# Optimization experiments

Measured on AMD Instinct MI355X. Metric: run time of the kernel, lower is better.

The kernel has to match this reference:

```python
import jax, jax.numpy as jnp
import numpy as np

NUM_CLASSES = 19  # number of distinct labels in targets (fill_max)


def setup_inputs() -> dict:
    key = jax.random.key(0)
    k1, k2 = jax.random.split(key)
    n, d = 262144, 128
    inputs = jax.random.normal(k1, (n, d), dtype=jnp.float32)
    targets = jax.random.randint(k2, (n,), 0, NUM_CLASSES, dtype=jnp.int64)
    return {"inputs": inputs, "targets": targets}


def reference(inputs, targets):
    # Same math as the O(n^2) torch loop: for each sample i, the center is the
    # mean of all samples sharing targets[i]. Computed as one segment-reduction
    # over labels followed by a gather.
    n = inputs.shape[0]
    sums = jax.ops.segment_sum(inputs, targets, num_segments=NUM_CLASSES)          # [C, d]
    counts = jax.ops.segment_sum(jnp.ones((n,), inputs.dtype), targets,
                                 num_segments=NUM_CLASSES)                          # [C]
    class_centers = sums / counts[:, None]                                          # [C, d]
    centers = class_centers[targets]                                                # [n, d]
    dist_pc = jnp.sqrt(jnp.sum((inputs - centers) ** 2, axis=1))                    # [n]
    return jnp.mean(dist_pc)
```

## Files before the change

kernel.cpp:

```cpp
#include <hip/hip_runtime.h>
#include <math.h>

#define NCLS 19
#define DIM  128
#define CD   (NCLS * DIM)
#define WPB  8
#define NBLK 256
#define NTHR 512
#define NWAVES (NBLK * WPB)
#define NRP  32

typedef float f32x4 __attribute__((ext_vector_type(4)));

__device__ __forceinline__ float4 ntload4(const float4* p) {
    f32x4 r = __builtin_nontemporal_load((const f32x4*)p);
    return make_float4(r.x, r.y, r.z, r.w);
}

template <int CTRL, int RMASK>
__device__ __forceinline__ float dpp_add(float x) {
    int t = __builtin_amdgcn_update_dpp(0, __builtin_bit_cast(int, x),
                                        CTRL, RMASK, 0xf, true);
    return x + __builtin_bit_cast(float, t);
}
__device__ __forceinline__ float reduce32_dpp(float x) {
    x = dpp_add<0x111, 0xf>(x);
    x = dpp_add<0x112, 0xf>(x);
    x = dpp_add<0x114, 0xf>(x);
    x = dpp_add<0x118, 0xf>(x);
    x = dpp_add<0x142, 0xa>(x);
    return x;
}

__device__ __forceinline__ void proc_pair(float* __restrict__ tbl,
                                          int* __restrict__ cnt,
                                          float4 v, int ca, int cb,
                                          int lane, int l31) {
    if (ca == cb) {
        v.x += __shfl_xor(v.x, 32, 64);
        v.y += __shfl_xor(v.y, 32, 64);
        v.z += __shfl_xor(v.z, 32, 64);
        v.w += __shfl_xor(v.w, 32, 64);
        float4* q = (float4*)&tbl[ca * DIM + l31 * 4];
        float4 a = *q;
        a.x += v.x; a.y += v.y; a.z += v.z; a.w += v.w;
        *q = a;
        if (lane == 0) cnt[ca] += 2;
    } else {
        int c = (lane >= 32) ? cb : ca;
        float4* q = (float4*)&tbl[c * DIM + l31 * 4];
        float4 a = *q;
        a.x += v.x; a.y += v.y; a.z += v.z; a.w += v.w;
        *q = a;
        if (lane == 0)  cnt[ca]++;
        if (lane == 32) cnt[cb]++;
    }
}

__global__ __launch_bounds__(NTHR, 2)
void k_fused(const float4* __restrict__ in4, const int* __restrict__ tgt,
             float* __restrict__ gsums, int* __restrict__ gcounts,
             int* __restrict__ bar, float* __restrict__ out,
             int npair, float inv_n) {
    __shared__ __align__(16) float ls[WPB * CD];
    __shared__ int   lcnt[WPB * NCLS];
    __shared__ __align__(16) float lcent[CD];
    __shared__ float red[NTHR];

    const int tid  = threadIdx.x;
    const int w    = tid >> 6;
    const int lane = tid & 63;
    const int l31  = lane & 31;
    float* tbl = &ls[w * CD];
    int*   cnt = &lcnt[w * NCLS];
    const int g = blockIdx.x * WPB + w;

    for (int i = tid; i < WPB * CD; i += NTHR) ls[i] = 0.0f;
    for (int i = tid; i < WPB * NCLS; i += NTHR) lcnt[i] = 0;
    __syncthreads();

    const int hstop = (npair >= NRP * NWAVES) ? NRP * NWAVES : 0;
    const bool full = hstop != 0;

    float4 hold[NRP];
    if (full) {
        #pragma unroll
        for (int k = 0; k < NRP; k += 4) {
            const int p0 = (k + 0) * NWAVES + g;
            const int p1 = (k + 1) * NWAVES + g;
            const int p2 = (k + 2) * NWAVES + g;
            const int p3 = (k + 3) * NWAVES + g;
            float4 v0 = ntload4(&in4[(size_t)p0 * 64 + lane]);
            float4 v1 = ntload4(&in4[(size_t)p1 * 64 + lane]);
            float4 v2 = ntload4(&in4[(size_t)p2 * 64 + lane]);
            float4 v3 = ntload4(&in4[(size_t)p3 * 64 + lane]);
            hold[k + 0] = v0; hold[k + 1] = v1;
            hold[k + 2] = v2; hold[k + 3] = v3;
            int a0 = tgt[2 * p0];  int b0 = tgt[2 * p0 + 1];
            int a1 = tgt[2 * p1];  int b1 = tgt[2 * p1 + 1];
            int a2 = tgt[2 * p2];  int b2 = tgt[2 * p2 + 1];
            int a3 = tgt[2 * p3];  int b3 = tgt[2 * p3 + 1];
            proc_pair(tbl, cnt, v0, a0, b0, lane, l31);
            proc_pair(tbl, cnt, v1, a1, b1, lane, l31);
            proc_pair(tbl, cnt, v2, a2, b2, lane, l31);
            proc_pair(tbl, cnt, v3, a3, b3, lane, l31);
        }
        #pragma unroll
        for (int k = 0; k < NRP; k++) {
            asm volatile("" : "+v"(hold[k].x), "+v"(hold[k].y),
                              "+v"(hold[k].z), "+v"(hold[k].w));
        }
    }

    int p = hstop + g;
    for (; p + 3 * NWAVES < npair; p += 4 * NWAVES) {
        float4 v0 = in4[(size_t)(p             ) * 64 + lane];
        float4 v1 = in4[(size_t)(p +     NWAVES) * 64 + lane];
        float4 v2 = in4[(size_t)(p + 2 * NWAVES) * 64 + lane];
        float4 v3 = in4[(size_t)(p + 3 * NWAVES) * 64 + lane];
        int a0 = tgt[2 * p];                  int b0 = tgt[2 * p + 1];
        int a1 = tgt[2 * (p + NWAVES)];       int b1 = tgt[2 * (p + NWAVES) + 1];
        int a2 = tgt[2 * (p + 2 * NWAVES)];   int b2 = tgt[2 * (p + 2 * NWAVES) + 1];
        int a3 = tgt[2 * (p + 3 * NWAVES)];   int b3 = tgt[2 * (p + 3 * NWAVES) + 1];
        proc_pair(tbl, cnt, v0, a0, b0, lane, l31);
        proc_pair(tbl, cnt, v1, a1, b1, lane, l31);
        proc_pair(tbl, cnt, v2, a2, b2, lane, l31);
        proc_pair(tbl, cnt, v3, a3, b3, lane, l31);
    }
    for (; p < npair; p += NWAVES) {
        float4 v = in4[(size_t)p * 64 + lane];
        int ca = tgt[2 * p];
        int cb = tgt[2 * p + 1];
        proc_pair(tbl, cnt, v, ca, cb, lane, l31);
    }
    __syncthreads();

    for (int i = tid; i < CD; i += NTHR) {
        float s = 0.0f;
        #pragma unroll
        for (int ww = 0; ww < WPB; ww++) s += ls[ww * CD + i];
        unsafeAtomicAdd(&gsums[i], s);
    }
    if (tid < NCLS) {
        int s = 0;
        #pragma unroll
        for (int ww = 0; ww < WPB; ww++) s += lcnt[ww * NCLS + tid];
        atomicAdd(&gcounts[tid], s);
    }

    __syncthreads();
    if (tid == 0) {
        __hip_atomic_fetch_add(bar, 1, __ATOMIC_ACQ_REL,
                               __HIP_MEMORY_SCOPE_AGENT);
        while (__hip_atomic_load(bar, __ATOMIC_ACQUIRE,
                                 __HIP_MEMORY_SCOPE_AGENT) < NBLK) {
            __builtin_amdgcn_s_sleep(8);
        }
    }
    __syncthreads();

    for (int i = tid; i < CD; i += NTHR) {
        float s = __hip_atomic_load(&gsums[i], __ATOMIC_RELAXED,
                                    __HIP_MEMORY_SCOPE_AGENT);
        int   c = __hip_atomic_load(&gcounts[i >> 7], __ATOMIC_RELAXED,
                                    __HIP_MEMORY_SCOPE_AGENT);
        lcent[i] = s / (float)c;
    }
    __syncthreads();

    float acc = 0.0f;

    if (full) {
        #pragma unroll
        for (int k = 0; k < NRP; k++) {
            const int pk = k * NWAVES + g;
            const int2 cc = *(const int2*)&tgt[2 * pk];
            const int c = (lane >= 32) ? cc.y : cc.x;
            const float4 e = *(const float4*)&lcent[c * DIM + l31 * 4];
            const float4 v = hold[k];
            float dx = v.x - e.x, dy = v.y - e.y;
            float dz = v.z - e.z, dw = v.w - e.w;
            float d = dx * dx + dy * dy + dz * dz + dw * dw;
            d = reduce32_dpp(d);
            if (l31 == 31) acc += sqrtf(d);
        }
    }

    int q = hstop + g;
    for (; q + NWAVES < npair; q += 2 * NWAVES) {
        float4 va = in4[(size_t)q * 64 + lane];
        float4 vb = in4[(size_t)(q + NWAVES) * 64 + lane];
        int2 c2a = *(const int2*)&tgt[2 * q];
        int2 c2b = *(const int2*)&tgt[2 * (q + NWAVES)];
        int ca = (lane >= 32) ? c2a.y : c2a.x;
        int cb = (lane >= 32) ? c2b.y : c2b.x;
        float4 ea = *(const float4*)&lcent[ca * DIM + l31 * 4];
        float4 eb = *(const float4*)&lcent[cb * DIM + l31 * 4];
        float dx, dy, dz, dw;
        dx = va.x - ea.x; dy = va.y - ea.y; dz = va.z - ea.z; dw = va.w - ea.w;
        float d0 = dx * dx + dy * dy + dz * dz + dw * dw;
        dx = vb.x - eb.x; dy = vb.y - eb.y; dz = vb.z - eb.z; dw = vb.w - eb.w;
        float d1 = dx * dx + dy * dy + dz * dz + dw * dw;
        d0 = reduce32_dpp(d0);
        d1 = reduce32_dpp(d1);
        if (l31 == 31) acc += sqrtf(d0) + sqrtf(d1);
    }
    for (; q < npair; q += NWAVES) {
        float4 v = in4[(size_t)q * 64 + lane];
        int2 c2 = *(const int2*)&tgt[2 * q];
        int c = (lane >= 32) ? c2.y : c2.x;
        float4 e = *(const float4*)&lcent[c * DIM + l31 * 4];
        float dx = v.x - e.x, dy = v.y - e.y, dz = v.z - e.z, dw = v.w - e.w;
        float d = dx * dx + dy * dy + dz * dz + dw * dw;
        d = reduce32_dpp(d);
        if (l31 == 31) acc += sqrtf(d);
    }

    red[tid] = acc;
    __syncthreads();
    for (int s = NTHR / 2; s > 0; s >>= 1) {
        if (tid < s) red[tid] += red[tid + s];
        __syncthreads();
    }
    if (tid == 0) unsafeAtomicAdd(out, red[0] * inv_n);
}

extern "C" void kernel_launch(void* const* d_in, const int* in_sizes, int n_in,
                              void* d_out, int out_size, void* d_ws, size_t ws_size,
                              hipStream_t stream) {
    const float* in  = (const float*)d_in[0];
    const int*   tgt = (const int*)d_in[1];
    const int n = in_sizes[0] / DIM;

    float* gsums   = (float*)d_ws;
    int*   gcounts = (int*)(gsums + CD);
    int*   bar     = gcounts + NCLS;
    float* out     = (float*)d_out;

    (void)hipMemsetAsync(d_ws, 0, (CD + NCLS + 1) * sizeof(float), stream);
    (void)hipMemsetAsync(d_out, 0, sizeof(float), stream);

    const float4* in4 = (const float4*)in;
    k_fused<<<NBLK, NTHR, 0, stream>>>(in4, tgt, gsums, gcounts, bar,
                                       out, n / 2, 1.0f / (float)n);
}
```

Before: 230.1 us.

## Share one LDS atomic table per block and cache extra pairs in LDS

Replaces the eight per-wave shared class-sum tables with one block-wide table updated by LDS float atomics. This removes the cross-wave merge step and frees shared memory. The freed space, plus more, holds 16 extra row-pairs per wave in LDS between the accumulation and distance phases, so the second pass rereads less input from global memory. Lanes now write to the sum table with a strided column layout, and the distance phase reads it back the same way. The costs are atomic contention on the shared table, more LDS instructions per pair, and about 150 KB of shared memory per block, which caps residency at one block per CU.

```diff
diff --git a/kernel.cpp b/kernel.cpp
--- a/kernel.cpp
+++ b/kernel.cpp
@@ -9,6 +9,8 @@
 #define NTHR 512
 #define NWAVES (NBLK * WPB)
 #define NRP  32
+#define NLP  16
+#define PPW  64
 
 typedef float f32x4 __attribute__((ext_vector_type(4)));
 
@@ -32,29 +34,27 @@
     return x;
 }
 
-__device__ __forceinline__ void proc_pair(float* __restrict__ tbl,
-                                          int* __restrict__ cnt,
-                                          float4 v, int ca, int cb,
-                                          int lane, int l31) {
-    if (ca == cb) {
-        v.x += __shfl_xor(v.x, 32, 64);
-        v.y += __shfl_xor(v.y, 32, 64);
-        v.z += __shfl_xor(v.z, 32, 64);
-        v.w += __shfl_xor(v.w, 32, 64);
-        float4* q = (float4*)&tbl[ca * DIM + l31 * 4];
-        float4 a = *q;
-        a.x += v.x; a.y += v.y; a.z += v.z; a.w += v.w;
-        *q = a;
-        if (lane == 0) cnt[ca] += 2;
-    } else {
-        int c = (lane >= 32) ? cb : ca;
-        float4* q = (float4*)&tbl[c * DIM + l31 * 4];
-        float4 a = *q;
-        a.x += v.x; a.y += v.y; a.z += v.z; a.w += v.w;
-        *q = a;
-        if (lane == 0)  cnt[ca]++;
-        if (lane == 32) cnt[cb]++;
-    }
+__device__ __forceinline__ void acc_pair(float* __restrict__ tbl,
+                                         int* __restrict__ cnt,
+                                         float4 v, int ca, int cb,
+                                         int lane, int l31) {
+    const int c = (lane >= 32) ? cb : ca;
+    float* row = &tbl[c * DIM];
+    atomicAdd(&row[l31     ], v.x);
+    atomicAdd(&row[l31 + 32], v.y);
+    atomicAdd(&row[l31 + 64], v.z);
+    atomicAdd(&row[l31 + 96], v.w);
+    if (l31 == 0) atomicAdd(&cnt[c], 1);
+}
+
+__device__ __forceinline__ float pair_dist2(const float* __restrict__ lcent,
+                                            float4 v, int c, int l31) {
+    const float* row = &lcent[c * DIM];
+    float dx = v.x - row[l31     ];
+    float dy = v.y - row[l31 + 32];
+    float dz = v.z - row[l31 + 64];
+    float dw = v.w - row[l31 + 96];
+    return dx * dx + dy * dy + dz * dz + dw * dw;
 }
 
 __global__ __launch_bounds__(NTHR, 2)
@@ -62,28 +62,27 @@
              float* __restrict__ gsums, int* __restrict__ gcounts,
              int* __restrict__ bar, float* __restrict__ out,
              int npair, float inv_n) {
-    __shared__ __align__(16) float ls[WPB * CD];
-    __shared__ int   lcnt[WPB * NCLS];
+    __shared__ __align__(16) float tbl[CD];
     __shared__ __align__(16) float lcent[CD];
+    __shared__ int   cnt[NCLS];
     __shared__ float red[NTHR];
+    __shared__ __align__(16) float4 holdl[WPB * NLP * 64];
 
     const int tid  = threadIdx.x;
     const int w    = tid >> 6;
     const int lane = tid & 63;
     const int l31  = lane & 31;
-    float* tbl = &ls[w * CD];
-    int*   cnt = &lcnt[w * NCLS];
-    const int g = blockIdx.x * WPB + w;
-
-    for (int i = tid; i < WPB * CD; i += NTHR) ls[i] = 0.0f;
-    for (int i = tid; i < WPB * NCLS; i += NTHR) lcnt[i] = 0;
-    __syncthreads();
-
-    const int hstop = (npair >= NRP * NWAVES) ? NRP * NWAVES : 0;
-    const bool full = hstop != 0;
+    const int g    = blockIdx.x * WPB + w;
+
+    for (int i = tid; i < CD; i += NTHR) tbl[i] = 0.0f;
+    if (tid < NCLS) cnt[tid] = 0;
+    __syncthreads();
+
+    const bool exact = (npair == PPW * NWAVES);
+    const int  lstop = exact ? (NRP + NLP) * NWAVES : 0;
 
     float4 hold[NRP];
-    if (full) {
+    if (exact) {
         #pragma unroll
         for (int k = 0; k < NRP; k += 4) {
             const int p0 = (k + 0) * NWAVES + g;
@@ -94,59 +93,75 @@
             float4 v1 = ntload4(&in4[(size_t)p1 * 64 + lane]);
             float4 v2 = ntload4(&in4[(size_t)p2 * 64 + lane]);
             float4 v3 = ntload4(&in4[(size_t)p3 * 64 + lane]);
+            int2 ab0 = *(const int2*)&tgt[2 * p0];
+            int2 ab1 = *(const int2*)&tgt[2 * p1];
+            int2 ab2 = *(const int2*)&tgt[2 * p2];
+            int2 ab3 = *(const int2*)&tgt[2 * p3];
             hold[k + 0] = v0; hold[k + 1] = v1;
             hold[k + 2] = v2; hold[k + 3] = v3;
-            int a0 = tgt[2 * p0];  int b0 = tgt[2 * p0 + 1];
-            int a1 = tgt[2 * p1];  int b1 = tgt[2 * p1 + 1];
-            int a2 = tgt[2 * p2];  int b2 = tgt[2 * p2 + 1];
-            int a3 = tgt[2 * p3];  int b3 = tgt[2 * p3 + 1];
-            proc_pair(tbl, cnt, v0, a0, b0, lane, l31);
-            proc_pair(tbl, cnt, v1, a1, b1, lane, l31);
-            proc_pair(tbl, cnt, v2, a2, b2, lane, l31);
-            proc_pair(tbl, cnt, v3, a3, b3, lane, l31);
+            acc_pair(tbl, cnt, v0, ab0.x, ab0.y, lane, l31);
+            acc_pair(tbl, cnt, v1, ab1.x, ab1.y, lane, l31);
+            acc_pair(tbl, cnt, v2, ab2.x, ab2.y, lane, l31);
+            acc_pair(tbl, cnt, v3, ab3.x, ab3.y, lane, l31);
         }
         #pragma unroll
         for (int k = 0; k < NRP; k++) {
             asm volatile("" : "+v"(hold[k].x), "+v"(hold[k].y),
                               "+v"(hold[k].z), "+v"(hold[k].w));
         }
-    }
-
-    int p = hstop + g;
+
+        float4* hbase = &holdl[(size_t)(w * NLP) * 64 + lane];
+        #pragma unroll
+        for (int k = 0; k < NLP; k += 4) {
+            const int p0 = (NRP + k + 0) * NWAVES + g;
+            const int p1 = (NRP + k + 1) * NWAVES + g;
+            const int p2 = (NRP + k + 2) * NWAVES + g;
+            const int p3 = (NRP + k + 3) * NWAVES + g;
+            float4 v0 = ntload4(&in4[(size_t)p0 * 64 + lane]);
+            float4 v1 = ntload4(&in4[(size_t)p1 * 64 + lane]);
+            float4 v2 = ntload4(&in4[(size_t)p2 * 64 + lane]);
+            float4 v3 = ntload4(&in4[(size_t)p3 * 64 + lane]);
+            int2 ab0 = *(const int2*)&tgt[2 * p0];
+            int2 ab1 = *(const int2*)&tgt[2 * p1];
+            int2 ab2 = *(const int2*)&tgt[2 * p2];
+            int2 ab3 = *(const int2*)&tgt[2 * p3];
+            hbase[(k + 0) * 64] = v0;
+            hbase[(k + 1) * 64] = v1;
+            hbase[(k + 2) * 64] = v2;
+            hbase[(k + 3) * 64] = v3;
+            acc_pair(tbl, cnt, v0, ab0.x, ab0.y, lane, l31);
+            acc_pair(tbl, cnt, v1, ab1.x, ab1.y, lane, l31);
+            acc_pair(tbl, cnt, v2, ab2.x, ab2.y, lane, l31);
+            acc_pair(tbl, cnt, v3, ab3.x, ab3.y, lane, l31);
+        }
+    }
+
+    int p = lstop + g;
     for (; p + 3 * NWAVES < npair; p += 4 * NWAVES) {
         float4 v0 = in4[(size_t)(p             ) * 64 + lane];
         float4 v1 = in4[(size_t)(p +     NWAVES) * 64 + lane];
         float4 v2 = in4[(size_t)(p + 2 * NWAVES) * 64 + lane];
         float4 v3 = in4[(size_t)(p + 3 * NWAVES) * 64 + lane];
-        int a0 = tgt[2 * p];                  int b0 = tgt[2 * p + 1];
-        int a1 = tgt[2 * (p + NWAVES)];       int b1 = tgt[2 * (p + NWAVES) + 1];
-        int a2 = tgt[2 * (p + 2 * NWAVES)];   int b2 = tgt[2 * (p + 2 * NWAVES) + 1];
-        int a3 = tgt[2 * (p + 3 * NWAVES)];   int b3 = tgt[2 * (p + 3 * NWAVES) + 1];
-        proc_pair(tbl, cnt, v0, a0, b0, lane, l31);
-        proc_pair(tbl, cnt, v1, a1, b1, lane, l31);
-        proc_pair(tbl, cnt, v2, a2, b2, lane, l31);
-        proc_pair(tbl, cnt, v3, a3, b3, lane, l31);
+        int2 ab0 = *(const int2*)&tgt[2 * p];
+        int2 ab1 = *(const int2*)&tgt[2 * (p + NWAVES)];
+        int2 ab2 = *(const int2*)&tgt[2 * (p + 2 * NWAVES)];
+        int2 ab3 = *(const int2*)&tgt[2 * (p + 3 * NWAVES)];
+        acc_pair(tbl, cnt, v0, ab0.x, ab0.y, lane, l31);
+        acc_pair(tbl, cnt, v1, ab1.x, ab1.y, lane, l31);
+        acc_pair(tbl, cnt, v2, ab2.x, ab2.y, lane, l31);
+        acc_pair(tbl, cnt, v3, ab3.x, ab3.y, lane, l31);
     }
     for (; p < npair; p += NWAVES) {
         float4 v = in4[(size_t)p * 64 + lane];
-        int ca = tgt[2 * p];
-        int cb = tgt[2 * p + 1];
-        proc_pair(tbl, cnt, v, ca, cb, lane, l31);
-    }
-    __syncthreads();
-
-    for (int i = tid; i < CD; i += NTHR) {
-        float s = 0.0f;
-        #pragma unroll
-        for (int ww = 0; ww < WPB; ww++) s += ls[ww * CD + i];
-        unsafeAtomicAdd(&gsums[i], s);
-    }
-    if (tid < NCLS) {
-        int s = 0;
-        #pragma unroll
-        for (int ww = 0; ww < WPB; ww++) s += lcnt[ww * NCLS + tid];
-        atomicAdd(&gcounts[tid], s);
-    }
+        int2 ab = *(const int2*)&tgt[2 * p];
+        acc_pair(tbl, cnt, v, ab.x, ab.y, lane, l31);
+    }
+    __syncthreads();
+
+    for (int i = tid; i < CD; i += NTHR)
+        unsafeAtomicAdd(&gsums[i], tbl[i]);
+    if (tid < NCLS)
+        atomicAdd(&gcounts[tid], cnt[tid]);
 
     __syncthreads();
     if (tid == 0) {
@@ -170,23 +185,30 @@
 
     float acc = 0.0f;
 
-    if (full) {
+    if (exact) {
         #pragma unroll
         for (int k = 0; k < NRP; k++) {
             const int pk = k * NWAVES + g;
             const int2 cc = *(const int2*)&tgt[2 * pk];
             const int c = (lane >= 32) ? cc.y : cc.x;
-            const float4 e = *(const float4*)&lcent[c * DIM + l31 * 4];
-            const float4 v = hold[k];
-            float dx = v.x - e.x, dy = v.y - e.y;
-            float dz = v.z - e.z, dw = v.w - e.w;
-            float d = dx * dx + dy * dy + dz * dz + dw * dw;
+            float d = pair_dist2(lcent, hold[k], c, l31);
             d = reduce32_dpp(d);
             if (l31 == 31) acc += sqrtf(d);
         }
-    }
-
-    int q = hstop + g;
+        const float4* hbase = &holdl[(size_t)(w * NLP) * 64 + lane];
+        #pragma unroll
+        for (int k = 0; k < NLP; k++) {
+            const int pk = (NRP + k) * NWAVES + g;
+            const int2 cc = *(const int2*)&tgt[2 * pk];
+            const int c = (lane >= 32) ? cc.y : cc.x;
+            float4 v = hbase[k * 64];
+            float d = pair_dist2(lcent, v, c, l31);
+            d = reduce32_dpp(d);
+            if (l31 == 31) acc += sqrtf(d);
+        }
+    }
+
+    int q = lstop + g;
     for (; q + NWAVES < npair; q += 2 * NWAVES) {
         float4 va = in4[(size_t)q * 64 + lane];
         float4 vb = in4[(size_t)(q + NWAVES) * 64 + lane];
@@ -194,13 +216,8 @@
         int2 c2b = *(const int2*)&tgt[2 * (q + NWAVES)];
         int ca = (lane >= 32) ? c2a.y : c2a.x;
         int cb = (lane >= 32) ? c2b.y : c2b.x;
-        float4 ea = *(const float4*)&lcent[ca * DIM + l31 * 4];
-        float4 eb = *(const float4*)&lcent[cb * DIM + l31 * 4];
-        float dx, dy, dz, dw;
-        dx = va.x - ea.x; dy = va.y - ea.y; dz = va.z - ea.z; dw = va.w - ea.w;
-        float d0 = dx * dx + dy * dy + dz * dz + dw * dw;
-        dx = vb.x - eb.x; dy = vb.y - eb.y; dz = vb.z - eb.z; dw = vb.w - eb.w;
-        float d1 = dx * dx + dy * dy + dz * dz + dw * dw;
+        float d0 = pair_dist2(lcent, va, ca, l31);
+        float d1 = pair_dist2(lcent, vb, cb, l31);
         d0 = reduce32_dpp(d0);
         d1 = reduce32_dpp(d1);
         if (l31 == 31) acc += sqrtf(d0) + sqrtf(d1);
@@ -209,9 +226,7 @@
         float4 v = in4[(size_t)q * 64 + lane];
         int2 c2 = *(const int2*)&tgt[2 * q];
         int c = (lane >= 32) ? c2.y : c2.x;
-        float4 e = *(const float4*)&lcent[c * DIM + l31 * 4];
-        float dx = v.x - e.x, dy = v.y - e.y, dz = v.z - e.z, dw = v.w - e.w;
-        float d = dx * dx + dy * dy + dz * dz + dw * dw;
+        float d = pair_dist2(lcent, v, c, l31);
         d = reduce32_dpp(d);
         if (l31 == 31) acc += sqrtf(d);
     }
```

Result: slower. 359.1 us (+56.1%).

## Stage extra input rows in LDS to cut second-pass global rereads

Applied to the files above, without the earlier changes.

Adds an LDS buffer holding 8 more pairs per wave beyond the 32 kept in registers, so 40 of the 64 pairs per wave skip the second global read after the grid barrier. To make room, the class-center table now reuses the per-wave sums LDS region instead of a separate array. Target labels are loaded as int2 pairs. The register/LDS path only runs when npair exactly matches the expected size, and the larger LDS footprint may reduce occupancy below 2 blocks per CU.

```diff
diff --git a/kernel.cpp b/kernel.cpp
--- a/kernel.cpp
+++ b/kernel.cpp
@@ -9,6 +9,8 @@
 #define NTHR 512
 #define NWAVES (NBLK * WPB)
 #define NRP  32
+#define NLP  8
+#define PPW  64
 
 typedef float f32x4 __attribute__((ext_vector_type(4)));
 
@@ -64,8 +66,8 @@
              int npair, float inv_n) {
     __shared__ __align__(16) float ls[WPB * CD];
     __shared__ int   lcnt[WPB * NCLS];
-    __shared__ __align__(16) float lcent[CD];
     __shared__ float red[NTHR];
+    __shared__ __align__(16) float4 holdl[WPB * NLP * 64];
 
     const int tid  = threadIdx.x;
     const int w    = tid >> 6;
@@ -79,11 +81,11 @@
     for (int i = tid; i < WPB * NCLS; i += NTHR) lcnt[i] = 0;
     __syncthreads();
 
-    const int hstop = (npair >= NRP * NWAVES) ? NRP * NWAVES : 0;
-    const bool full = hstop != 0;
+    const bool exact = (npair == PPW * NWAVES);
+    const int  lstop = exact ? (NRP + NLP) * NWAVES : 0;
 
     float4 hold[NRP];
-    if (full) {
+    if (exact) {
         #pragma unroll
         for (int k = 0; k < NRP; k += 4) {
             const int p0 = (k + 0) * NWAVES + g;
@@ -94,44 +96,68 @@
             float4 v1 = ntload4(&in4[(size_t)p1 * 64 + lane]);
             float4 v2 = ntload4(&in4[(size_t)p2 * 64 + lane]);
             float4 v3 = ntload4(&in4[(size_t)p3 * 64 + lane]);
+            int2 ab0 = *(const int2*)&tgt[2 * p0];
+            int2 ab1 = *(const int2*)&tgt[2 * p1];
+            int2 ab2 = *(const int2*)&tgt[2 * p2];
+            int2 ab3 = *(const int2*)&tgt[2 * p3];
             hold[k + 0] = v0; hold[k + 1] = v1;
             hold[k + 2] = v2; hold[k + 3] = v3;
-            int a0 = tgt[2 * p0];  int b0 = tgt[2 * p0 + 1];
-            int a1 = tgt[2 * p1];  int b1 = tgt[2 * p1 + 1];
-            int a2 = tgt[2 * p2];  int b2 = tgt[2 * p2 + 1];
-            int a3 = tgt[2 * p3];  int b3 = tgt[2 * p3 + 1];
-            proc_pair(tbl, cnt, v0, a0, b0, lane, l31);
-            proc_pair(tbl, cnt, v1, a1, b1, lane, l31);
-            proc_pair(tbl, cnt, v2, a2, b2, lane, l31);
-            proc_pair(tbl, cnt, v3, a3, b3, lane, l31);
+            proc_pair(tbl, cnt, v0, ab0.x, ab0.y, lane, l31);
+            proc_pair(tbl, cnt, v1, ab1.x, ab1.y, lane, l31);
+            proc_pair(tbl, cnt, v2, ab2.x, ab2.y, lane, l31);
+            proc_pair(tbl, cnt, v3, ab3.x, ab3.y, lane, l31);
         }
         #pragma unroll
         for (int k = 0; k < NRP; k++) {
             asm volatile("" : "+v"(hold[k].x), "+v"(hold[k].y),
                               "+v"(hold[k].z), "+v"(hold[k].w));
         }
-    }
-
-    int p = hstop + g;
+
+        float4* hbase = &holdl[(size_t)(w * NLP) * 64 + lane];
+        #pragma unroll
+        for (int k = 0; k < NLP; k += 4) {
+            const int p0 = (NRP + k + 0) * NWAVES + g;
+            const int p1 = (NRP + k + 1) * NWAVES + g;
+            const int p2 = (NRP + k + 2) * NWAVES + g;
+            const int p3 = (NRP + k + 3) * NWAVES + g;
+            float4 v0 = ntload4(&in4[(size_t)p0 * 64 + lane]);
+            float4 v1 = ntload4(&in4[(size_t)p1 * 64 + lane]);
+            float4 v2 = ntload4(&in4[(size_t)p2 * 64 + lane]);
+            float4 v3 = ntload4(&in4[(size_t)p3 * 64 + lane]);
+            int2 ab0 = *(const int2*)&tgt[2 * p0];
+            int2 ab1 = *(const int2*)&tgt[2 * p1];
+            int2 ab2 = *(const int2*)&tgt[2 * p2];
+            int2 ab3 = *(const int2*)&tgt[2 * p3];
+            hbase[(k + 0) * 64] = v0;
+            hbase[(k + 1) * 64] = v1;
+            hbase[(k + 2) * 64] = v2;
+            hbase[(k + 3) * 64] = v3;
+            proc_pair(tbl, cnt, v0, ab0.x, ab0.y, lane, l31);
+            proc_pair(tbl, cnt, v1, ab1.x, ab1.y, lane, l31);
+            proc_pair(tbl, cnt, v2, ab2.x, ab2.y, lane, l31);
+            proc_pair(tbl, cnt, v3, ab3.x, ab3.y, lane, l31);
+        }
+    }
+
+    int p = lstop + g;
     for (; p + 3 * NWAVES < npair; p += 4 * NWAVES) {
         float4 v0 = in4[(size_t)(p             ) * 64 + lane];
         float4 v1 = in4[(size_t)(p +     NWAVES) * 64 + lane];
         float4 v2 = in4[(size_t)(p + 2 * NWAVES) * 64 + lane];
         float4 v3 = in4[(size_t)(p + 3 * NWAVES) * 64 + lane];
-        int a0 = tgt[2 * p];                  int b0 = tgt[2 * p + 1];
-        int a1 = tgt[2 * (p + NWAVES)];       int b1 = tgt[2 * (p + NWAVES) + 1];
-        int a2 = tgt[2 * (p + 2 * NWAVES)];   int b2 = tgt[2 * (p + 2 * NWAVES) + 1];
-        int a3 = tgt[2 * (p + 3 * NWAVES)];   int b3 = tgt[2 * (p + 3 * NWAVES) + 1];
-        proc_pair(tbl, cnt, v0, a0, b0, lane, l31);
-        proc_pair(tbl, cnt, v1, a1, b1, lane, l31);
-        proc_pair(tbl, cnt, v2, a2, b2, lane, l31);
-        proc_pair(tbl, cnt, v3, a3, b3, lane, l31);
+        int2 ab0 = *(const int2*)&tgt[2 * p];
+        int2 ab1 = *(const int2*)&tgt[2 * (p + NWAVES)];
+        int2 ab2 = *(const int2*)&tgt[2 * (p + 2 * NWAVES)];
+        int2 ab3 = *(const int2*)&tgt[2 * (p + 3 * NWAVES)];
+        proc_pair(tbl, cnt, v0, ab0.x, ab0.y, lane, l31);
+        proc_pair(tbl, cnt, v1, ab1.x, ab1.y, lane, l31);
+        proc_pair(tbl, cnt, v2, ab2.x, ab2.y, lane, l31);
+        proc_pair(tbl, cnt, v3, ab3.x, ab3.y, lane, l31);
     }
     for (; p < npair; p += NWAVES) {
         float4 v = in4[(size_t)p * 64 + lane];
-        int ca = tgt[2 * p];
-        int cb = tgt[2 * p + 1];
-        proc_pair(tbl, cnt, v, ca, cb, lane, l31);
+        int2 ab = *(const int2*)&tgt[2 * p];
+        proc_pair(tbl, cnt, v, ab.x, ab.y, lane, l31);
     }
     __syncthreads();
 
@@ -159,6 +185,7 @@
     }
     __syncthreads();
 
+    float* lcent = ls;
     for (int i = tid; i < CD; i += NTHR) {
         float s = __hip_atomic_load(&gsums[i], __ATOMIC_RELAXED,
                                     __HIP_MEMORY_SCOPE_AGENT);
@@ -170,7 +197,7 @@
 
     float acc = 0.0f;
 
-    if (full) {
+    if (exact) {
         #pragma unroll
         for (int k = 0; k < NRP; k++) {
             const int pk = k * NWAVES + g;
@@ -184,9 +211,23 @@
             d = reduce32_dpp(d);
             if (l31 == 31) acc += sqrtf(d);
         }
-    }
-
-    int q = hstop + g;
+        const float4* hbase = &holdl[(size_t)(w * NLP) * 64 + lane];
+        #pragma unroll
+        for (int k = 0; k < NLP; k++) {
+            const int pk = (NRP + k) * NWAVES + g;
+            const int2 cc = *(const int2*)&tgt[2 * pk];
+            const int c = (lane >= 32) ? cc.y : cc.x;
+            float4 v = hbase[k * 64];
+            const float4 e = *(const float4*)&lcent[c * DIM + l31 * 4];
+            float dx = v.x - e.x, dy = v.y - e.y;
+            float dz = v.z - e.z, dw = v.w - e.w;
+            float d = dx * dx + dy * dy + dz * dz + dw * dw;
+            d = reduce32_dpp(d);
+            if (l31 == 31) acc += sqrtf(d);
+        }
+    }
+
+    int q = lstop + g;
     for (; q + NWAVES < npair; q += 2 * NWAVES) {
         float4 va = in4[(size_t)q * 64 + lane];
         float4 vb = in4[(size_t)(q + NWAVES) * 64 + lane];
@@ -194,8 +235,8 @@
         int2 c2b = *(const int2*)&tgt[2 * (q + NWAVES)];
         int ca = (lane >= 32) ? c2a.y : c2a.x;
         int cb = (lane >= 32) ? c2b.y : c2b.x;
-        float4 ea = *(const float4*)&lcent[ca * DIM + l31 * 4];
-        float4 eb = *(const float4*)&lcent[cb * DIM + l31 * 4];
+        const float4 ea = *(const float4*)&lcent[ca * DIM + l31 * 4];
+        const float4 eb = *(const float4*)&lcent[cb * DIM + l31 * 4];
         float dx, dy, dz, dw;
         dx = va.x - ea.x; dy = va.y - ea.y; dz = va.z - ea.z; dw = va.w - ea.w;
         float d0 = dx * dx + dy * dy + dz * dz + dw * dw;
@@ -209,7 +250,7 @@
         float4 v = in4[(size_t)q * 64 + lane];
         int2 c2 = *(const int2*)&tgt[2 * q];
         int c = (lane >= 32) ? c2.y : c2.x;
-        float4 e = *(const float4*)&lcent[c * DIM + l31 * 4];
+        const float4 e = *(const float4*)&lcent[c * DIM + l31 * 4];
         float dx = v.x - e.x, dy = v.y - e.y, dz = v.z - e.z, dw = v.w - e.w;
         float d = dx * dx + dy * dy + dz * dz + dw * dw;
         d = reduce32_dpp(d);
```

Measured after the change: 230.3 us. About the same (+0.1%).
